# Kernel tuning notes

Hardware: AMD Instinct MI355X
Metric: run time of the kernel (lower is better)

Reference implementation:

```python
import jax, jax.numpy as jnp
import numpy as np


def _gcn_conv(x, edge_index, W, b):
    """PyG GCNConv: add self-loops, symmetric normalization, scatter-add aggregation."""
    N = x.shape[0]
    loops = jnp.arange(N, dtype=edge_index.dtype)
    src = jnp.concatenate([edge_index[0], loops])  # [E+N]
    dst = jnp.concatenate([edge_index[1], loops])  # [E+N]
    # degree computed on destination nodes (flow: source_to_target)
    deg = jax.ops.segment_sum(jnp.ones_like(dst, dtype=x.dtype), dst, num_segments=N)
    deg_inv_sqrt = jnp.where(deg > 0, jax.lax.rsqrt(jnp.maximum(deg, 1.0)), 0.0)
    norm = deg_inv_sqrt[src] * deg_inv_sqrt[dst]  # [E+N]
    h = x @ W  # [N, out]
    msg = h[src] * norm[:, None]  # [E+N, out]
    out = jax.ops.segment_sum(msg, dst, num_segments=N)
    return out + b


def setup_inputs() -> dict:
    key = jax.random.key(0)
    k1, k2, k3, k4 = jax.random.split(key, 4)
    N, E, D_IN, D_HID, D_OUT = 100000, 1600000, 128, 128, 64
    x = jax.random.normal(k1, (N, D_IN), dtype=jnp.float32)
    edge_index = jax.random.randint(k2, (2, E), 0, N, dtype=jnp.int64)
    batch = jnp.zeros((N,), dtype=jnp.int64)
    W1 = jax.random.normal(k3, (D_IN, D_HID), dtype=jnp.float32) / np.sqrt(D_IN)
    b1 = jnp.zeros((D_HID,), dtype=jnp.float32)
    W2 = jax.random.normal(k4, (D_HID, D_OUT), dtype=jnp.float32) / np.sqrt(D_HID)
    b2 = jnp.zeros((D_OUT,), dtype=jnp.float32)
    return {"x": x, "edge_index": edge_index, "batch": batch,
            "W1": W1, "b1": b1, "W2": W2, "b2": b2}


def reference(x, edge_index, batch, W1, b1, W2, b2):
    h = _gcn_conv(x, edge_index, W1, b1)
    h = jax.nn.relu(h)
    # dropout is identity at inference (training=False)
    out = _gcn_conv(h, edge_index, W2, b2)
    # original computes F.log_softmax but discards it; returns out
    return out
```

## Files before the change

kernel.cpp:

```cpp
#include <hip/hip_runtime.h>
#include <hip/hip_fp16.h>


#define KDIM 128
#define BSHIFT 9
#define BSIZE 512
#define ECHUNK 2048
#define CAP 10240
#define PACK_SHIFT 20
#define PACK_MASK ((1u << PACK_SHIFT) - 1)

typedef _Float16 h8 __attribute__((ext_vector_type(8)));
typedef float f4v __attribute__((ext_vector_type(4)));


__launch_bounds__(256) __global__
void bscatter_kernel(const int* __restrict__ src, const int* __restrict__ dst,
                     int* __restrict__ ecnt, unsigned int* __restrict__ packed_out,
                     int E, int NB) {
    __shared__ int lcnt[256];
    __shared__ int lexc[256];
    __shared__ int lbase[256];
    __shared__ unsigned int lpacked[ECHUNK];
    __shared__ unsigned char lbslot[ECHUNK];

    const int t = threadIdx.x;
    lcnt[t] = 0;
    __syncthreads();

    const int base = blockIdx.x * ECHUNK;
    const int cnt = min(ECHUNK, E - base);

#pragma unroll
    for (int j = 0; j < ECHUNK / 256; j++) {
        int e = base + j * 256 + t;
        if (e < E) atomicAdd(&lcnt[dst[e] >> BSHIFT], 1);
    }
    __syncthreads();

    lexc[t] = lcnt[t];
    __syncthreads();
    for (int off = 1; off < 256; off <<= 1) {
        int x = (t >= off) ? lexc[t - off] : 0;
        __syncthreads();
        if (t >= off) lexc[t] += x;
        __syncthreads();
    }
    lexc[t] = lexc[t] - lcnt[t];

    if (t < NB && lcnt[t]) lbase[t] = t * CAP + atomicAdd(&ecnt[t], lcnt[t]);
    __syncthreads();
    lcnt[t] = lexc[t];
    __syncthreads();

#pragma unroll
    for (int j = 0; j < ECHUNK / 256; j++) {
        int e = base + j * 256 + t;
        if (e < E) {
            int d = dst[e];
            int b = d >> BSHIFT;
            int pos = atomicAdd(&lcnt[b], 1);
            lpacked[pos] = (unsigned int)src[e] | ((unsigned int)(d & (BSIZE - 1)) << PACK_SHIFT);
            lbslot[pos] = (unsigned char)b;
        }
    }
    __syncthreads();

#pragma unroll
    for (int j = 0; j < ECHUNK / 256; j++) {
        int s = j * 256 + t;
        if (s < cnt) {
            int b = lbslot[s];
            int pos = lbase[b] + (s - lexc[b]);
            if (pos < (b + 1) * CAP)
                packed_out[pos] = lpacked[s];
        }
    }
}


__launch_bounds__(1024) __global__
void bfinal_kernel(const unsigned int* __restrict__ packed, const int* __restrict__ ecnt,
                   int* __restrict__ rowptr, float* __restrict__ dinv,
                   int* __restrict__ ssrc, int N, int E, int NB) {
    __shared__ int ncnt[BSIZE];
    __shared__ int sbuf[BSIZE];
    __shared__ int bsc[256];
    __shared__ int bbase_sh;

    const int t = threadIdx.x;
    const int b = blockIdx.x;

    if (t < 256) bsc[t] = (t < NB) ? min(ecnt[t], CAP) : 0;
    if (t < BSIZE) ncnt[t] = 0;
    __syncthreads();

    const int cnt = min(ecnt[b], CAP);
    const unsigned int* pb = packed + (size_t)b * CAP;
    unsigned int held[CAP / 1024];
#pragma unroll
    for (int j = 0; j < CAP / 1024; j++) {
        int e = t + j * 1024;
        if (e < cnt) {
            unsigned int p = pb[e];
            held[j] = p;
            atomicAdd(&ncnt[p >> PACK_SHIFT], 1);
        }
    }

    __syncthreads();
    for (int off = 1; off < 256; off <<= 1) {
        int x = 0;
        if (t < 256 && t >= off) x = bsc[t - off];
        __syncthreads();
        if (t < 256 && t >= off) bsc[t] += x;
        __syncthreads();
    }
    if (t == 0) bbase_sh = (b == 0) ? 0 : bsc[b - 1];

    int mycnt = 0;
    if (t < BSIZE) {
        mycnt = ncnt[t];
        sbuf[t] = mycnt;
    }
    __syncthreads();
    for (int off = 1; off < BSIZE; off <<= 1) {
        int x = 0;
        if (t < BSIZE && t >= off) x = sbuf[t - off];
        __syncthreads();
        if (t < BSIZE && t >= off) sbuf[t] += x;
        __syncthreads();
    }

    const int gb = bbase_sh;
    if (t < BSIZE) {
        int exc = (t == 0) ? 0 : sbuf[t - 1];
        int node = (b << BSHIFT) + t;
        if (node < N) {
            rowptr[node] = gb + exc;
            dinv[node] = rsqrtf((float)(mycnt + 1));
        }
        ncnt[t] = gb + exc;
    }
    if (t == 0 && b == NB - 1) rowptr[N] = gb + cnt;
    __syncthreads();

#pragma unroll
    for (int j = 0; j < CAP / 1024; j++) {
        int e = t + j * 1024;
        if (e < cnt) {
            unsigned int p = held[j];
            int d = p >> PACK_SHIFT;
            int pos = atomicAdd(&ncnt[d], 1);
            ssrc[pos] = (int)(p & PACK_MASK);
        }
    }
}


__device__ inline h8 pack8(float4 u, float4 v) {
    h8 r;
    r[0] = (_Float16)u.x; r[1] = (_Float16)u.y; r[2] = (_Float16)u.z; r[3] = (_Float16)u.w;
    r[4] = (_Float16)v.x; r[5] = (_Float16)v.y; r[6] = (_Float16)v.z; r[7] = (_Float16)v.w;
    return r;
}

template <int DOUT, bool AHALF>
__launch_bounds__(256) __global__
void gemm_mfma_kernel(const void* __restrict__ Xv, const float* __restrict__ W,
                      const float* __restrict__ dinv, _Float16* __restrict__ outh, int N) {
    constexpr int K = KDIM;
    constexpr int KS = K + 8;
    constexpr int NT = DOUT / 16;
    __shared__ _Float16 Wl[DOUT * KS];

    const int t = threadIdx.x;
    const int wave = t >> 6;
    const int lane = t & 63;
    const int l15 = lane & 15;
    const int quad = lane >> 4;

#pragma unroll
    for (int i = t; i < DOUT * (K / 4); i += 256) {
        int n = i & (DOUT - 1);
        int kg = i / DOUT;
        union { _Float16 h[4]; uint2 u; } tmp;
#pragma unroll
        for (int j = 0; j < 4; j++)
            tmp.h[j] = (_Float16)W[(size_t)(kg * 4 + j) * DOUT + n];
        *(uint2*)(&Wl[n * KS + kg * 4]) = tmp.u;
    }
    __syncthreads();

    const int rowbase = blockIdx.x * 128;
    const int row0 = rowbase + wave * 32 + l15;
    const int row1 = row0 + 16;
    const int rc0 = min(row0, N - 1);
    const int rc1 = min(row1, N - 1);

    f4v acc[2][NT];
#pragma unroll
    for (int r = 0; r < 2; r++)
#pragma unroll
        for (int ct = 0; ct < NT; ct++) acc[r][ct] = (f4v)0.0f;

#pragma unroll
    for (int kc = 0; kc < K; kc += 32) {
        const int kof = kc + quad * 8;
        h8 a0, a1;
        if (AHALF) {
            const _Float16* Xh = (const _Float16*)Xv;
            a0 = *(const h8*)(Xh + (size_t)rc0 * K + kof);
            a1 = *(const h8*)(Xh + (size_t)rc1 * K + kof);
        } else {
            const float* Xf = (const float*)Xv;
            const float* p0 = Xf + (size_t)rc0 * K + kof;
            const float* p1 = Xf + (size_t)rc1 * K + kof;
            a0 = pack8(*(const float4*)p0, *(const float4*)(p0 + 4));
            a1 = pack8(*(const float4*)p1, *(const float4*)(p1 + 4));
        }
#pragma unroll
        for (int ct = 0; ct < NT; ct++) {
            h8 b = *(const h8*)(&Wl[(size_t)(ct * 16 + l15) * KS + kof]);
            acc[0][ct] = __builtin_amdgcn_mfma_f32_16x16x32_f16(a0, b, acc[0][ct], 0, 0, 0);
            acc[1][ct] = __builtin_amdgcn_mfma_f32_16x16x32_f16(a1, b, acc[1][ct], 0, 0, 0);
        }
    }

#pragma unroll
    for (int r = 0; r < 2; r++) {
        const int rb = rowbase + wave * 32 + r * 16 + quad * 4;
#pragma unroll
        for (int g = 0; g < 4; g++) {
            int row = rb + g;
            if (row < N) {
                float di = dinv[row];
                _Float16* op = outh + (size_t)row * DOUT + l15;
#pragma unroll
                for (int ct = 0; ct < NT; ct++)
                    op[ct * 16] = (_Float16)(acc[r][ct][g] * di);
            }
        }
    }
}


__launch_bounds__(256) __global__
void agg_gemm_kernel(const __half* __restrict__ hs, const int* __restrict__ rowptr,
                     const int* __restrict__ ssrc, const float* __restrict__ dinv,
                     const float* __restrict__ bias, const float* __restrict__ W2,
                     _Float16* __restrict__ hs2, int N) {
    constexpr int K = KDIM;
    constexpr int KS = K + 8;
    constexpr int DO2 = 64;
    __shared__ _Float16 W2l[DO2 * KS];
    __shared__ _Float16 o_lds[16 * KS];

    const int t = threadIdx.x;

#pragma unroll
    for (int i = t; i < DO2 * (K / 4); i += 256) {
        int n = i & (DO2 - 1);
        int kg = i / DO2;
        union { _Float16 h[4]; uint2 u; } tmp;
#pragma unroll
        for (int j = 0; j < 4; j++)
            tmp.h[j] = (_Float16)W2[(size_t)(kg * 4 + j) * DO2 + n];
        *(uint2*)(&W2l[n * KS + kg * 4]) = tmp.u;
    }

    const int nl = t >> 4;
    const int node = blockIdx.x * 16 + nl;
    const int flane = t & 15;
    const int c0 = flane * 8;

    h8 oh;
    if (node < N) {
        float acc[8];
        {
            uint4 u = *(const uint4*)(hs + (size_t)node * K + c0);
            const __half2* hp = (const __half2*)&u;
#pragma unroll
            for (int q = 0; q < 4; q++) {
                float2 f = __half22float2(hp[q]);
                acc[2 * q] = f.x;
                acc[2 * q + 1] = f.y;
            }
        }

        const int e0 = rowptr[node];
        const int e1 = rowptr[node + 1];
        int e = e0;
        for (; e + 4 <= e1; e += 4) {
            int s0 = ssrc[e + 0];
            int s1 = ssrc[e + 1];
            int s2 = ssrc[e + 2];
            int s3 = ssrc[e + 3];
            uint4 u0 = *(const uint4*)(hs + (size_t)s0 * K + c0);
            uint4 u1 = *(const uint4*)(hs + (size_t)s1 * K + c0);
            uint4 u2 = *(const uint4*)(hs + (size_t)s2 * K + c0);
            uint4 u3 = *(const uint4*)(hs + (size_t)s3 * K + c0);
            const __half2* p0 = (const __half2*)&u0;
            const __half2* p1 = (const __half2*)&u1;
            const __half2* p2 = (const __half2*)&u2;
            const __half2* p3 = (const __half2*)&u3;
#pragma unroll
            for (int q = 0; q < 4; q++) {
                float2 f0 = __half22float2(p0[q]);
                float2 f1 = __half22float2(p1[q]);
                float2 f2 = __half22float2(p2[q]);
                float2 f3 = __half22float2(p3[q]);
                acc[2 * q]     += (f0.x + f1.x) + (f2.x + f3.x);
                acc[2 * q + 1] += (f0.y + f1.y) + (f2.y + f3.y);
            }
        }
        for (; e < e1; e++) {
            int s = ssrc[e];
            uint4 u = *(const uint4*)(hs + (size_t)s * K + c0);
            const __half2* hp = (const __half2*)&u;
#pragma unroll
            for (int q = 0; q < 4; q++) {
                float2 f = __half22float2(hp[q]);
                acc[2 * q] += f.x;
                acc[2 * q + 1] += f.y;
            }
        }

        const float di = dinv[node];
#pragma unroll
        for (int q = 0; q < 2; q++) {
            float4 bq = *(const float4*)(bias + c0 + 4 * q);
            float o0 = fmaxf(di * acc[4 * q + 0] + bq.x, 0.f);
            float o1 = fmaxf(di * acc[4 * q + 1] + bq.y, 0.f);
            float o2 = fmaxf(di * acc[4 * q + 2] + bq.z, 0.f);
            float o3 = fmaxf(di * acc[4 * q + 3] + bq.w, 0.f);
            oh[4 * q + 0] = (_Float16)o0;
            oh[4 * q + 1] = (_Float16)o1;
            oh[4 * q + 2] = (_Float16)o2;
            oh[4 * q + 3] = (_Float16)o3;
        }
    } else {
#pragma unroll
        for (int j = 0; j < 8; j++) oh[j] = (_Float16)0.f;
    }

    *(h8*)(&o_lds[nl * KS + c0]) = oh;
    __syncthreads();

    const int wv = t >> 6;
    const int l15 = t & 15;
    const int quad = (t & 63) >> 4;

    f4v a2 = (f4v)0.0f;
#pragma unroll
    for (int kc = 0; kc < K; kc += 32) {
        const int kof = kc + quad * 8;
        h8 a = *(const h8*)(&o_lds[l15 * KS + kof]);
        h8 b = *(const h8*)(&W2l[(size_t)(wv * 16 + l15) * KS + kof]);
        a2 = __builtin_amdgcn_mfma_f32_16x16x32_f16(a, b, a2, 0, 0, 0);
    }

    const int rowbase = blockIdx.x * 16;
#pragma unroll
    for (int g = 0; g < 4; g++) {
        int r = rowbase + quad * 4 + g;
        if (r < N)
            hs2[(size_t)r * DO2 + wv * 16 + l15] = (_Float16)(a2[g] * dinv[r]);
    }
}


template <int DOUT, bool RELU, bool HOUT>
__launch_bounds__(256) __global__
void agg_kernel(const __half* __restrict__ hs, const int* __restrict__ rowptr,
                const int* __restrict__ ssrc, const float* __restrict__ dinv,
                const float* __restrict__ bias, void* __restrict__ outv, int N) {
    constexpr int TPN = DOUT / 8;
    const int npb = blockDim.x / TPN;
    const int node = blockIdx.x * npb + threadIdx.x / TPN;
    if (node >= N) return;
    const int lane = threadIdx.x % TPN;
    const int c0 = lane * 8;

    float acc[8];
    {
        uint4 u = *(const uint4*)(hs + (size_t)node * DOUT + c0);
        const __half2* hp = (const __half2*)&u;
#pragma unroll
        for (int q = 0; q < 4; q++) {
            float2 f = __half22float2(hp[q]);
            acc[2 * q] = f.x;
            acc[2 * q + 1] = f.y;
        }
    }

    const int e0 = rowptr[node];
    const int e1 = rowptr[node + 1];
    int e = e0;
    for (; e + 4 <= e1; e += 4) {
        int s0 = ssrc[e + 0];
        int s1 = ssrc[e + 1];
        int s2 = ssrc[e + 2];
        int s3 = ssrc[e + 3];
        uint4 u0 = *(const uint4*)(hs + (size_t)s0 * DOUT + c0);
        uint4 u1 = *(const uint4*)(hs + (size_t)s1 * DOUT + c0);
        uint4 u2 = *(const uint4*)(hs + (size_t)s2 * DOUT + c0);
        uint4 u3 = *(const uint4*)(hs + (size_t)s3 * DOUT + c0);
        const __half2* p0 = (const __half2*)&u0;
        const __half2* p1 = (const __half2*)&u1;
        const __half2* p2 = (const __half2*)&u2;
        const __half2* p3 = (const __half2*)&u3;
#pragma unroll
        for (int q = 0; q < 4; q++) {
            float2 f0 = __half22float2(p0[q]);
            float2 f1 = __half22float2(p1[q]);
            float2 f2 = __half22float2(p2[q]);
            float2 f3 = __half22float2(p3[q]);
            acc[2 * q]     += (f0.x + f1.x) + (f2.x + f3.x);
            acc[2 * q + 1] += (f0.y + f1.y) + (f2.y + f3.y);
        }
    }
    for (; e < e1; e++) {
        int s = ssrc[e];
        uint4 u = *(const uint4*)(hs + (size_t)s * DOUT + c0);
        const __half2* hp = (const __half2*)&u;
#pragma unroll
        for (int q = 0; q < 4; q++) {
            float2 f = __half22float2(hp[q]);
            acc[2 * q] += f.x;
            acc[2 * q + 1] += f.y;
        }
    }

    const float di = dinv[node];
    float o[8];
#pragma unroll
    for (int q = 0; q < 2; q++) {
        float4 bq = *(const float4*)(bias + c0 + 4 * q);
        o[4 * q + 0] = di * acc[4 * q + 0] + bq.x;
        o[4 * q + 1] = di * acc[4 * q + 1] + bq.y;
        o[4 * q + 2] = di * acc[4 * q + 2] + bq.z;
        o[4 * q + 3] = di * acc[4 * q + 3] + bq.w;
    }
    if (RELU) {
#pragma unroll
        for (int j = 0; j < 8; j++) o[j] = fmaxf(o[j], 0.f);
    }
    if (HOUT) {
        union { __half2 h[4]; uint4 u; } pk;
#pragma unroll
        for (int q = 0; q < 4; q++)
            pk.h[q] = __floats2half2_rn(o[2 * q], o[2 * q + 1]);
        *(uint4*)((__half*)outv + (size_t)node * DOUT + c0) = pk.u;
    } else {
        float* op = (float*)outv + (size_t)node * DOUT + c0;
        *(float4*)op = make_float4(o[0], o[1], o[2], o[3]);
        *(float4*)(op + 4) = make_float4(o[4], o[5], o[6], o[7]);
    }
}


extern "C" void kernel_launch(void* const* d_in, const int* in_sizes, int n_in,
                              void* d_out, int out_size, void* d_ws, size_t ws_size,
                              hipStream_t stream) {
    const float* x  = (const float*)d_in[0];
    const int*   ei = (const int*)d_in[1];
    const float* W1 = (const float*)d_in[3];
    const float* b1 = (const float*)d_in[4];
    const float* W2 = (const float*)d_in[5];
    const float* b2 = (const float*)d_in[6];
    float* out = (float*)d_out;

    const int N = in_sizes[0] / KDIM;
    const int E = in_sizes[1] / 2;
    const int* esrc = ei;
    const int* edst = ei + E;
    const int NB = (N + BSIZE - 1) >> BSHIFT;

    char* ws = (char*)d_ws;
    size_t off = 0;
    auto alloc = [&](size_t bytes) {
        size_t p = off;
        off = (off + bytes + 511) & ~(size_t)511;
        return p;
    };
    int*      ecnt    = (int*)(ws + alloc((size_t)NB * 4));
    int*      rowptr  = (int*)(ws + alloc((size_t)(N + 1) * 4));
    float*    dinv    = (float*)(ws + alloc((size_t)N * 4));
    int*      ssrc    = (int*)(ws + alloc((size_t)E * 4));
    _Float16* hs1     = (_Float16*)(ws + alloc((size_t)N * KDIM * 2));
    _Float16* hs2     = (_Float16*)(ws + alloc((size_t)N * 64 * 2));
    unsigned int* packed = (unsigned int*)hs1;
    (void)ws_size; (void)n_in; (void)out_size;

    const int eb = (E + ECHUNK - 1) / ECHUNK;

    hipMemsetAsync(ecnt, 0, (size_t)NB * 4, stream);

    bscatter_kernel<<<eb, 256, 0, stream>>>(esrc, edst, ecnt, packed, E, NB);
    bfinal_kernel<<<NB, 1024, 0, stream>>>(packed, ecnt, rowptr, dinv, ssrc, N, E, NB);

    gemm_mfma_kernel<128, false><<<(N + 127) / 128, 256, 0, stream>>>(x, W1, dinv, hs1, N);

    agg_gemm_kernel<<<(N + 15) / 16, 256, 0, stream>>>(
        (const __half*)hs1, rowptr, ssrc, dinv, b1, W2, hs2, N);

    agg_kernel<64, false, false><<<(N + 31) / 32, 256, 0, stream>>>(
        (const __half*)hs2, rowptr, ssrc, dinv, b2, out, N);
}
```

Baseline: 261.5 us.

## Make agg_gemm wave-local with 32 nodes per block and no post-gather barrier

Blocks in the fused aggregate+GEMM kernel grow to 512 threads covering 32 nodes. Each wave now stages only its own 4 aggregated rows in a private LDS slice and runs the W2 MFMAs for those rows itself, so the block-wide __syncthreads between the gather and the GEMM is gone. This also halves how often W2 is loaded and converted into LDS per node. The cost is wasted MFMA work, since 16-row tiles carry only 4 distinct rows and each wave issues four times as many MFMAs. It also adds a hand-placed lgkmcnt wait and a sched_barrier.

```diff
diff --git a/kernel.cpp b/kernel.cpp
--- a/kernel.cpp
+++ b/kernel.cpp
@@ -245,7 +245,7 @@
 }
 
 
-__launch_bounds__(256) __global__
+__launch_bounds__(512, 8) __global__
 void agg_gemm_kernel(const __half* __restrict__ hs, const int* __restrict__ rowptr,
                      const int* __restrict__ ssrc, const float* __restrict__ dinv,
                      const float* __restrict__ bias, const float* __restrict__ W2,
@@ -254,23 +254,24 @@
     constexpr int KS = K + 8;
     constexpr int DO2 = 64;
     __shared__ _Float16 W2l[DO2 * KS];
-    __shared__ _Float16 o_lds[16 * KS];
+    __shared__ _Float16 o_lds[8][4 * KS];
 
     const int t = threadIdx.x;
 
 #pragma unroll
-    for (int i = t; i < DO2 * (K / 4); i += 256) {
+    for (int i = t; i < DO2 * (K / 4); i += 512) {
         int n = i & (DO2 - 1);
-        int kg = i / DO2;
+        int kg = i >> 6;
         union { _Float16 h[4]; uint2 u; } tmp;
 #pragma unroll
         for (int j = 0; j < 4; j++)
             tmp.h[j] = (_Float16)W2[(size_t)(kg * 4 + j) * DO2 + n];
         *(uint2*)(&W2l[n * KS + kg * 4]) = tmp.u;
     }
+    __syncthreads();
 
     const int nl = t >> 4;
-    const int node = blockIdx.x * 16 + nl;
+    const int node = blockIdx.x * 32 + nl;
     const int flane = t & 15;
     const int c0 = flane * 8;
 
@@ -330,42 +331,49 @@
 #pragma unroll
         for (int q = 0; q < 2; q++) {
             float4 bq = *(const float4*)(bias + c0 + 4 * q);
-            float o0 = fmaxf(di * acc[4 * q + 0] + bq.x, 0.f);
-            float o1 = fmaxf(di * acc[4 * q + 1] + bq.y, 0.f);
-            float o2 = fmaxf(di * acc[4 * q + 2] + bq.z, 0.f);
-            float o3 = fmaxf(di * acc[4 * q + 3] + bq.w, 0.f);
-            oh[4 * q + 0] = (_Float16)o0;
-            oh[4 * q + 1] = (_Float16)o1;
-            oh[4 * q + 2] = (_Float16)o2;
-            oh[4 * q + 3] = (_Float16)o3;
+            oh[4 * q + 0] = (_Float16)fmaxf(di * acc[4 * q + 0] + bq.x, 0.f);
+            oh[4 * q + 1] = (_Float16)fmaxf(di * acc[4 * q + 1] + bq.y, 0.f);
+            oh[4 * q + 2] = (_Float16)fmaxf(di * acc[4 * q + 2] + bq.z, 0.f);
+            oh[4 * q + 3] = (_Float16)fmaxf(di * acc[4 * q + 3] + bq.w, 0.f);
         }
     } else {
 #pragma unroll
         for (int j = 0; j < 8; j++) oh[j] = (_Float16)0.f;
     }
 
-    *(h8*)(&o_lds[nl * KS + c0]) = oh;
-    __syncthreads();
-
     const int wv = t >> 6;
-    const int l15 = t & 15;
-    const int quad = (t & 63) >> 4;
-
-    f4v a2 = (f4v)0.0f;
+    const int a = (t >> 4) & 3;
+    *(h8*)(&o_lds[wv][a * KS + c0]) = oh;
+    asm volatile("s_waitcnt lgkmcnt(0)" ::: "memory");
+    __builtin_amdgcn_sched_barrier(0);
+
+    const int lane = t & 63;
+    const int l15 = lane & 15;
+    const int quad = lane >> 4;
+
+    f4v acc2[4];
+#pragma unroll
+    for (int ct = 0; ct < 4; ct++) acc2[ct] = (f4v)0.0f;
+
 #pragma unroll
     for (int kc = 0; kc < K; kc += 32) {
         const int kof = kc + quad * 8;
-        h8 a = *(const h8*)(&o_lds[l15 * KS + kof]);
-        h8 b = *(const h8*)(&W2l[(size_t)(wv * 16 + l15) * KS + kof]);
-        a2 = __builtin_amdgcn_mfma_f32_16x16x32_f16(a, b, a2, 0, 0, 0);
-    }
-
-    const int rowbase = blockIdx.x * 16;
+        h8 afr = *(const h8*)(&o_lds[wv][(l15 & 3) * KS + kof]);
+#pragma unroll
+        for (int ct = 0; ct < 4; ct++) {
+            h8 b = *(const h8*)(&W2l[(size_t)(ct * 16 + l15) * KS + kof]);
+            acc2[ct] = __builtin_amdgcn_mfma_f32_16x16x32_f16(afr, b, acc2[ct], 0, 0, 0);
+        }
+    }
+
+    f4v av = (quad == 0) ? acc2[0] : (quad == 1) ? acc2[1]
+           : (quad == 2) ? acc2[2] : acc2[3];
+    const int rowbase = blockIdx.x * 32 + wv * 4;
 #pragma unroll
     for (int g = 0; g < 4; g++) {
-        int r = rowbase + quad * 4 + g;
+        int r = rowbase + g;
         if (r < N)
-            hs2[(size_t)r * DO2 + wv * 16 + l15] = (_Float16)(a2[g] * dinv[r]);
+            hs2[(size_t)r * DO2 + quad * 16 + l15] = (_Float16)(av[g] * dinv[r]);
     }
 }
 
@@ -502,7 +510,7 @@
 
     gemm_mfma_kernel<128, false><<<(N + 127) / 128, 256, 0, stream>>>(x, W1, dinv, hs1, N);
 
-    agg_gemm_kernel<<<(N + 15) / 16, 256, 0, stream>>>(
+    agg_gemm_kernel<<<(N + 31) / 32, 512, 0, stream>>>(
         (const __half*)hs1, rowptr, ssrc, dinv, b1, W2, hs2, N);
 
     agg_kernel<64, false, false><<<(N + 31) / 32, 256, 0, stream>>>(
```

New measurement: 254.8 us. 2.6% less time.
